# Performance work log

Measured on AMD Instinct MI355X. Metric: run time of the kernel, lower is better.

The kernel has to match this reference:

```python
import jax, jax.numpy as jnp
import numpy as np

S = 3      # num_scales
CIN = 3    # in_channels (hardcoded by expand(...,3,...) in source)
COUT = 3   # out_channels (forced by final broadcast)
K = 3
PAD = 1


def setup_inputs() -> dict:
    key = jax.random.key(0)
    ks = jax.random.split(key, 8)
    B, H, W = 4, 384, 384
    x = jax.random.normal(ks[0], (B, CIN, H, W), jnp.float32)
    # params follow the torch inits: theta,sigma ~ U(0,pi); f0,theta0 = 1
    theta = jax.random.uniform(ks[1], (S, COUT, CIN), jnp.float32) * jnp.pi
    sigma = jax.random.uniform(ks[2], (S, COUT, CIN), jnp.float32) * jnp.pi
    f0 = jnp.ones((S, COUT, CIN), jnp.float32)
    theta0 = jnp.ones((S, COUT, CIN), jnp.float32)
    attn_w1 = jax.random.normal(ks[3], (64, CIN), jnp.float32) * 0.1     # 1x1 conv weight
    attn_b1 = jnp.zeros((64,), jnp.float32)
    attn_w2 = jax.random.normal(ks[4], (COUT * S, 64), jnp.float32) * 0.1
    attn_b2 = jnp.zeros((COUT * S,), jnp.float32)
    conv_w = jax.random.normal(ks[5], (COUT, CIN, K, K), jnp.float32) * 0.05
    mixing = jax.random.uniform(ks[6], (1,), jnp.float32)
    band = jax.random.uniform(ks[7], (COUT, CIN, 2), jnp.float32)        # freq_band_select ~ U(0,1)
    return dict(x=x, theta=theta, sigma=sigma, f0=f0, theta0=theta0,
                attn_w1=attn_w1, attn_b1=attn_b1, attn_w2=attn_w2, attn_b2=attn_b2,
                conv_w=conv_w, mixing=mixing, band=band)


def _log_gabor_bank(theta, sigma, f0, theta0, H, W):
    # vectorized over all scales: returns [S, Co, Cin, H, W] real filter bank
    yy, xx = jnp.meshgrid(jnp.linspace(-1.0, 1.0, H), jnp.linspace(-1.0, 1.0, W), indexing='ij')
    r = jnp.sqrt(xx * xx + yy * yy + 1e-6)          # [H,W]
    phi = jnp.arctan2(yy, xx)                        # [H,W]
    f0e = f0[..., None, None]                        # [S,Co,Cin,1,1]
    sig = sigma[..., None, None]
    th = theta[..., None, None]
    th0 = theta0[..., None, None]
    log_gabor = jnp.exp(-jnp.log(r - jnp.log(f0e)) ** 2 / (2.0 * jnp.log(sig) ** 2))
    angular = jnp.exp(-(phi - th) ** 2 / (2.0 * th0 ** 2))
    return log_gabor * angular


def _forward(x, theta, sigma, f0, theta0, attn_w1, attn_b1, attn_w2, attn_b2, conv_w, mixing, band):
    B, Cin, H, W = x.shape
    # torch.fft.fftshift with no dim shifts ALL axes (incl. batch/channel) -- replicate exactly
    x_freq_shift = jnp.fft.fftshift(jnp.fft.fft2(x))                 # [B,Cin,H,W] complex64

    filt = _log_gabor_bank(theta, sigma, f0, theta0, H, W)           # [S,Co,Cin,H,W]

    # attention net: 1x1 conv -> relu -> 1x1 conv -> softmax over channel dim
    mag = jnp.abs(x_freq_shift)
    h1 = jax.nn.relu(jnp.einsum('bchw,oc->bohw', mag, attn_w1) + attn_b1[None, :, None, None])
    logits = jnp.einsum('bchw,oc->bohw', h1, attn_w2) + attn_b2[None, :, None, None]
    attn = jax.nn.softmax(logits, axis=1).reshape(B, S, COUT, H, W)

    # attended[b,d,h,w] = sum_{s,co} attn[b,s,co,h,w] * xfreq[b,d,h,w] * filt[s,co,d,h,w]
    wgt = jnp.einsum('bschw,scdhw->bdhw', attn, filt)                # real [B,Cin,H,W]
    attended = (x_freq_shift * wgt).sum(axis=1)                      # [B,H,W] complex

    # per-(out,in)-channel square band mask, indices from height (as in source)
    start_idx = jnp.floor((band[..., 0] + 1.0) / 2.0 * H).astype(jnp.int32)   # [Co,Cin]
    end_idx = jnp.floor((band[..., 1] + 1.0) / 2.0 * H).astype(jnp.int32)
    ih = jnp.arange(H)
    rm = (ih[None, None, :] >= start_idx[..., None]) & (ih[None, None, :] < end_idx[..., None])
    iw = jnp.arange(W)
    cm = (iw[None, None, :] >= start_idx[..., None]) & (iw[None, None, :] < end_idx[..., None])
    mask = (rm[..., :, None] & cm[..., None, :]).astype(x.dtype)     # [Co,Cin,H,W]

    # broadcast quirk in source: [B,1,H,W] * [B,Co,1,Cin,H,W] -> [B,Co,B,Cin,H,W]
    six = mask[None, :, None, :, :, :] * attended[None, None, :, None, :, :]
    six = jnp.broadcast_to(six, (B, COUT, B, Cin, H, W))
    # torch ifftshift with no dim shifts ALL 6 axes; ifft2 transforms last two
    x_filtered = jnp.fft.ifft2(jnp.fft.ifftshift(six)).real          # [B,Co,B,Cin,H,W]

    x_spatial = jax.lax.conv_general_dilated(
        x, conv_w, window_strides=(1, 1), padding=[(PAD, PAD), (PAD, PAD)],
        dimension_numbers=('NCHW', 'OIHW', 'NCHW'))                  # [B,Co,H,W]

    mix = mixing[0]
    return mix * x_filtered + (1.0 - mix) * x_spatial[None, None]    # [B,Co,B,Cin,H,W]


def reference(x, theta, sigma, f0, theta0, attn_w1, attn_b1, attn_w2, attn_b2, conv_w, mixing, band):
    return _forward(x, theta, sigma, f0, theta0, attn_w1, attn_b1, attn_w2, attn_b2, conv_w, mixing, band)
```

## Files before the change

kernel.cpp:

```cpp
#include <hip/hip_runtime.h>
#include <math.h>

#define N384 384
#define NPIX 147456
#define LSTRIDE 385
#define LINES 8

__device__ __forceinline__ float2 cmul(float2 a, float2 b) {
    return make_float2(a.x*b.x - a.y*b.y, a.x*b.y + a.y*b.x);
}

template <int NT>
__device__ __forceinline__ void build_tw(float2* tw, int tid) {
    for (int k = tid; k < 384; k += NT) {
        float sn, cs;
        sincospif((float)k * (2.0f / 384.0f), &sn, &cs);
        tw[k] = make_float2(cs, sn);
    }
}

template <int SGNI>
__device__ float2* fft384x8(float2* b0, float2* b1, const float2* tw, int tid) {
    float2* src = b0;
    float2* dst = b1;
    const int line = tid >> 5;
    const int l32  = tid & 31;
    const float SG = (float)SGNI;
    const float s3 = SG * 0.86602540378443864676f;

    {
        float2* L = src + line * LSTRIDE;
        float2* D = dst + line * LSTRIDE;
#pragma unroll
        for (int q = 0; q < 2; ++q) {
            int i = l32 + 32 * q;
            float2 e0 = L[i],       e1 = L[i + 128], e2 = L[i + 256];
            float2 o0 = L[i + 64],  o1 = L[i + 192], o2 = L[i + 320];
            float t1x = e1.x + e2.x, t1y = e1.y + e2.y;
            float t2x = e1.x - e2.x, t2y = e1.y - e2.y;
            float2 E0 = make_float2(e0.x + t1x, e0.y + t1y);
            float mx = e0.x - 0.5f * t1x, my = e0.y - 0.5f * t1y;
            float ux = -s3 * t2y, uy = s3 * t2x;
            float2 E1 = make_float2(mx + ux, my + uy);
            float2 E2 = make_float2(mx - ux, my - uy);
            float s1x = o1.x + o2.x, s1y = o1.y + o2.y;
            float s2x = o1.x - o2.x, s2y = o1.y - o2.y;
            float2 O0 = make_float2(o0.x + s1x, o0.y + s1y);
            float nx = o0.x - 0.5f * s1x, ny = o0.y - 0.5f * s1y;
            float vx = -s3 * s2y, vy = s3 * s2x;
            float2 O1 = make_float2(nx + vx, ny + vy);
            float2 O2 = make_float2(nx - vx, ny - vy);
            float2 T1 = make_float2(0.5f * O1.x - s3 * O1.y, 0.5f * O1.y + s3 * O1.x);
            float2 T2 = make_float2(-0.5f * O2.x - s3 * O2.y, -0.5f * O2.y + s3 * O2.x);
            float2 y0 = make_float2(E0.x + O0.x, E0.y + O0.y);
            float2 y3 = make_float2(E0.x - O0.x, E0.y - O0.y);
            float2 y1 = make_float2(E1.x + T1.x, E1.y + T1.y);
            float2 y4 = make_float2(E1.x - T1.x, E1.y - T1.y);
            float2 y2 = make_float2(E2.x + T2.x, E2.y + T2.y);
            float2 y5 = make_float2(E2.x - T2.x, E2.y - T2.y);
            float2 c1 = tw[i], c2 = tw[2 * i], c3 = tw[3 * i], c4 = tw[4 * i], c5 = tw[5 * i];
            int o = 6 * i;
            D[o]     = y0;
            D[o + 1] = cmul(y1, make_float2(c1.x, SG * c1.y));
            D[o + 2] = cmul(y2, make_float2(c2.x, SG * c2.y));
            D[o + 3] = cmul(y3, make_float2(c3.x, SG * c3.y));
            D[o + 4] = cmul(y4, make_float2(c4.x, SG * c4.y));
            D[o + 5] = cmul(y5, make_float2(c5.x, SG * c5.y));
        }
    }
    __syncthreads();
    { float2* t = src; src = dst; dst = t; }

#pragma unroll
    for (int st = 0; st < 2; ++st) {
        const int s = (st == 0) ? 6 : 24;
        float2* L = src + line * LSTRIDE;
        float2* D = dst + line * LSTRIDE;
#pragma unroll
        for (int q = 0; q < 3; ++q) {
            int i = l32 + 32 * q;
            int k = i % s;
            int js = i - k;
            float2 A0 = L[i];
            float2 A1 = L[i + 96];
            float2 A2 = L[i + 192];
            float2 A3 = L[i + 288];
            float t0x = A0.x + A2.x, t0y = A0.y + A2.y;
            float t1x = A0.x - A2.x, t1y = A0.y - A2.y;
            float t2x = A1.x + A3.x, t2y = A1.y + A3.y;
            float t3x = A1.x - A3.x, t3y = A1.y - A3.y;
            float u3x = -SG * t3y,   u3y = SG * t3x;
            float2 y0 = make_float2(t0x + t2x, t0y + t2y);
            float2 y2 = make_float2(t0x - t2x, t0y - t2y);
            float2 y1 = make_float2(t1x + u3x, t1y + u3y);
            float2 y3 = make_float2(t1x - u3x, t1y - u3y);
            float2 c1 = tw[js], c2 = tw[2 * js], c3 = tw[3 * js];
            float2 w1 = make_float2(c1.x, SG * c1.y);
            float2 w2 = make_float2(c2.x, SG * c2.y);
            float2 w3 = make_float2(c3.x, SG * c3.y);
            int o = i + 3 * js;
            D[o]         = y0;
            D[o + s]     = cmul(y1, w1);
            D[o + 2 * s] = cmul(y2, w2);
            D[o + 3 * s] = cmul(y3, w3);
        }
        __syncthreads();
        { float2* t = src; src = dst; dst = t; }
    }

    {
        float2* L = src + line * LSTRIDE;
        float2* D = dst + line * LSTRIDE;
#pragma unroll
        for (int q = 0; q < 3; ++q) {
            int i = l32 + 32 * q;
            float2 A0 = L[i];
            float2 A1 = L[i + 96];
            float2 A2 = L[i + 192];
            float2 A3 = L[i + 288];
            float t0x = A0.x + A2.x, t0y = A0.y + A2.y;
            float t1x = A0.x - A2.x, t1y = A0.y - A2.y;
            float t2x = A1.x + A3.x, t2y = A1.y + A3.y;
            float t3x = A1.x - A3.x, t3y = A1.y - A3.y;
            float u3x = -SG * t3y,   u3y = SG * t3x;
            D[i]       = make_float2(t0x + t2x, t0y + t2y);
            D[i + 96]  = make_float2(t1x + u3x, t1y + u3y);
            D[i + 192] = make_float2(t0x - t2x, t0y - t2y);
            D[i + 288] = make_float2(t1x - u3x, t1y - u3y);
        }
    }
    __syncthreads();
    return dst;
}

__global__ __launch_bounds__(256) void k_fwd_rows(const float* __restrict__ x,
                                                  float2* __restrict__ F1) {
    __shared__ float2 sbuf[2][LINES * LSTRIDE];
    __shared__ float2 tw[384];
    int img = blockIdx.y;
    int rg  = blockIdx.x;
    int tid = threadIdx.x;
    build_tw<256>(tw, tid);
    const float4* xim = (const float4*)(x + (size_t)img * NPIX + (size_t)rg * 16 * 384);
    for (int idx4 = tid; idx4 < 1536; idx4 += 256) {
        int row = idx4 / 96;
        int e   = (idx4 - row * 96) * 4;
        float4 v = xim[idx4];
        float* L = (float*)(sbuf[0] + (row >> 1) * LSTRIDE + e) + (row & 1);
        L[0] = v.x; L[2] = v.y; L[4] = v.z; L[6] = v.w;
    }
    __syncthreads();
    float2* res = fft384x8<-1>(sbuf[0], sbuf[1], tw, tid);
    float2* F1b = F1 + (size_t)img * NPIX + (size_t)rg * 16 * 384;
    for (int it = tid; it < 1536; it += 256) {
        int line = it / 192;
        int k2   = it - line * 192;
        const float2* L = res + line * LSTRIDE;
        float2 A = L[k2];
        int m = (k2 == 0) ? 0 : 384 - k2;
        float2 B = L[m];
        float2 X1 = make_float2(0.5f * (A.x + B.x), 0.5f * (A.y - B.y));
        float2 X2 = make_float2(0.5f * (A.y + B.y), 0.5f * (B.x - A.x));
        F1b[(size_t)(2 * line) * 384 + k2]     = X1;
        F1b[(size_t)(2 * line + 1) * 384 + k2] = X2;
    }
}

__global__ __launch_bounds__(256) void k_fwd_cols(const float2* __restrict__ In,
                                                  float2* __restrict__ Out) {
    __shared__ float2 sbuf[2][LINES * LSTRIDE];
    __shared__ float2 tw[384];
    int img = blockIdx.y;
    int cg  = blockIdx.x;
    int tid = threadIdx.x;
    build_tw<256>(tw, tid);
    const float4* inim = (const float4*)(In + (size_t)img * NPIX + cg * 8);
    int c = tid & 3, hb = tid >> 2;
    for (int q = 0; q < 6; ++q) {
        int h = hb + 64 * q;
        float4 v = inim[(size_t)h * 192 + c];
        sbuf[0][(2 * c) * LSTRIDE + h]     = make_float2(v.x, v.y);
        sbuf[0][(2 * c + 1) * LSTRIDE + h] = make_float2(v.z, v.w);
    }
    __syncthreads();
    float2* res = fft384x8<-1>(sbuf[0], sbuf[1], tw, tid);
    float4* outim = (float4*)(Out + (size_t)img * NPIX + cg * 8);
    for (int q = 0; q < 3; ++q) {
        int h = hb + 64 * q;
        float2 a = res[(2 * c) * LSTRIDE + h];
        float2 b = res[(2 * c + 1) * LSTRIDE + h];
        outim[(size_t)h * 192 + c] = make_float4(a.x, a.y, b.x, b.y);
    }
}

__global__ __launch_bounds__(192) void k_attn(const float2* __restrict__ F2,
                                              const float* __restrict__ theta,
                                              const float* __restrict__ sigma,
                                              const float* __restrict__ f0,
                                              const float* __restrict__ theta0,
                                              const float* __restrict__ aw1,
                                              const float* __restrict__ ab1,
                                              const float* __restrict__ aw2,
                                              const float* __restrict__ ab2,
                                              const float* __restrict__ band,
                                              float2* __restrict__ A) {
    __shared__ float4 par[27];
    int tid = threadIdx.x;
    if (tid < 27) {
        float lf0 = logf(f0[tid]);
        float ls  = logf(sigma[tid]);
        float na  = -0.5f / (ls * ls);
        float th  = theta[tid];
        float t0  = theta0[tid];
        float nb  = -0.5f / (t0 * t0);
        par[tid] = make_float4(lf0, na, th, nb);
    }
    __syncthreads();

    int h = 192 + blockIdx.x;
    int w = 192 + tid;

    bool needed = false;
#pragma unroll
    for (int q = 0; q < 9; ++q) {
        int s = (int)floorf((band[2 * q + 0] + 1.0f) * 0.5f * 384.0f);
        int e = (int)floorf((band[2 * q + 1] + 1.0f) * 0.5f * 384.0f);
        needed |= (h >= s) && (h < e) && (w >= s) && (w < e);
    }
    if (__ballot(needed) == 0ULL) return;

    int hs = h - 192;
    int ws = w - 192;

    float2 xf[4][3];
    float  mag[4][3];
#pragma unroll
    for (int b = 0; b < 4; ++b) {
        int bp = (b + 2) & 3;
#pragma unroll
        for (int c = 0; c < 3; ++c) {
            int cp = c + 2; if (cp >= 3) cp -= 3;
            float2 v = F2[(size_t)(bp * 3 + cp) * NPIX + (size_t)hs * 384 + ws];
            xf[b][c]  = v;
            mag[b][c] = sqrtf(v.x * v.x + v.y * v.y);
        }
    }

    float lgt[4][9];
#pragma unroll
    for (int b = 0; b < 4; ++b)
#pragma unroll
        for (int j = 0; j < 9; ++j) lgt[b][j] = ab2[j];
    for (int o = 0; o < 64; ++o) {
        float w0 = aw1[o * 3 + 0], w1 = aw1[o * 3 + 1], w2 = aw1[o * 3 + 2];
        float bb = ab1[o];
        float hv[4];
#pragma unroll
        for (int b = 0; b < 4; ++b)
            hv[b] = fmaxf(bb + w0 * mag[b][0] + w1 * mag[b][1] + w2 * mag[b][2], 0.0f);
#pragma unroll
        for (int j = 0; j < 9; ++j) {
            float wj = aw2[j * 64 + o];
#pragma unroll
            for (int b = 0; b < 4; ++b) lgt[b][j] += wj * hv[b];
        }
    }

    float yy = -1.0f + 2.0f * (float)h / 383.0f;
    float xx = -1.0f + 2.0f * (float)w / 383.0f;
    float r   = sqrtf(xx * xx + yy * yy + 1e-6f);
    float phi = atan2f(yy, xx);
    float filt[27];
#pragma unroll
    for (int i = 0; i < 27; ++i) {
        float4 pr = par[i];
        float lr = logf(r - pr.x);
        float dphi = phi - pr.z;
        filt[i] = expf(lr * lr * pr.y + dphi * dphi * pr.w);
    }

#pragma unroll
    for (int b = 0; b < 4; ++b) {
        float mxv = lgt[b][0];
#pragma unroll
        for (int j = 1; j < 9; ++j) mxv = fmaxf(mxv, lgt[b][j]);
        float e[9];
        float se = 0.0f;
#pragma unroll
        for (int j = 0; j < 9; ++j) { e[j] = expf(lgt[b][j] - mxv); se += e[j]; }
        float inv = 1.0f / se;

        float2 acc = make_float2(0.0f, 0.0f);
#pragma unroll
        for (int d = 0; d < 3; ++d) {
            float wg = 0.0f;
#pragma unroll
            for (int s = 0; s < 3; ++s)
#pragma unroll
                for (int co = 0; co < 3; ++co)
                    wg += e[s * 3 + co] * filt[(s * 3 + co) * 3 + d];
            wg *= inv;
            acc.x += xf[b][d].x * wg;
            acc.y += xf[b][d].y * wg;
        }
        if (needed)
            A[(size_t)b * NPIX + (size_t)h * 384 + w] = acc;
    }
}

__global__ __launch_bounds__(256) void k_masked_rows(const float2* __restrict__ A,
                                                     const float* __restrict__ band,
                                                     float2* __restrict__ G1c) {
    int ii  = blockIdx.y;
    int rg  = blockIdx.x;
    int cop = ii / 12;
    int bp  = (ii / 3) % 4;
    int dp  = ii % 3;
    int pidx = (cop * 3 + dp) * 2;
    int sidx = (int)floorf((band[pidx + 0] + 1.0f) * 0.5f * 384.0f);
    int eidx = (int)floorf((band[pidx + 1] + 1.0f) * 0.5f * 384.0f);
    if (eidx <= sidx) return;
    int h0 = 192 + rg * 8;
    if (h0 + 8 <= sidx || h0 >= eidx) return;

    __shared__ float2 sbuf[2][LINES * LSTRIDE];
    __shared__ float2 tw[384];
    int tid = threadIdx.x;
    build_tw<256>(tw, tid);
    const float2* Ab = A + (size_t)bp * NPIX;
    for (int idx = tid; idx < 8 * 384; idx += 256) {
        int line = idx / 384;
        int w    = idx - line * 384;
        int h    = h0 + line;
        bool m = (h >= sidx) && (h < eidx) && (w >= sidx) && (w < eidx);
        float2 v = make_float2(0.0f, 0.0f);
        if (m) v = Ab[(size_t)h * 384 + w];
        sbuf[0][line * LSTRIDE + w] = v;
    }
    __syncthreads();
    float2* res = fft384x8<1>(sbuf[0], sbuf[1], tw, tid);
    for (int idx = tid; idx < 8 * 384; idx += 256) {
        int line = idx / 384;
        int w    = idx - line * 384;
        int h    = h0 + line;
        if (h >= sidx && h < eidx) {
            float2 v = res[line * LSTRIDE + w];
            if (w & 1) { v.x = -v.x; v.y = -v.y; }
            G1c[((size_t)ii * 192 + (h - sidx)) * 384 + w] = v;
        }
    }
}

__global__ __launch_bounds__(128) void k_col_gemm_combine(const float2* __restrict__ G1c,
                                                          const float* __restrict__ band,
                                                          const float* __restrict__ x,
                                                          const float* __restrict__ cw,
                                                          const float* __restrict__ mixing,
                                                          float* __restrict__ out) {
    __shared__ float2 tw[384];
    int tid = threadIdx.x;
    build_tw<128>(tw, tid);

    int ii  = blockIdx.y;
    int gt  = blockIdx.x * 128 + tid;
    int wq  = gt % 96;
    int hg  = gt / 96;
    int w   = wq * 4;
    int h0  = hg * 4;

    int cop = ii / 12;
    int bp  = (ii / 3) % 4;
    int dp  = ii % 3;
    int pidx = (cop * 3 + dp) * 2;
    int sidx = (int)floorf((band[pidx + 0] + 1.0f) * 0.5f * 384.0f);
    int eidx = (int)floorf((band[pidx + 1] + 1.0f) * 0.5f * 384.0f);
    __syncthreads();

    float acc[4][4];
#pragma unroll
    for (int kh = 0; kh < 4; ++kh)
#pragma unroll
        for (int j = 0; j < 4; ++j) acc[kh][j] = 0.0f;

    float2 t[4], rot[4];
#pragma unroll
    for (int kh = 0; kh < 4; ++kh) {
        int h = h0 + kh;
        t[kh]   = tw[(sidx * h) % 384];
        rot[kh] = tw[h];
    }

    const float4* g = (const float4*)(G1c + (size_t)ii * 192 * 384 + w);
    for (int hp = sidx; hp < eidx; ++hp) {
        float4 g0 = g[(size_t)(hp - sidx) * 192];
        float4 g1 = g[(size_t)(hp - sidx) * 192 + 1];
#pragma unroll
        for (int kh = 0; kh < 4; ++kh) {
            float tx = t[kh].x, ty = t[kh].y;
            acc[kh][0] += tx * g0.x - ty * g0.y;
            acc[kh][1] += tx * g0.z - ty * g0.w;
            acc[kh][2] += tx * g1.x - ty * g1.y;
            acc[kh][3] += tx * g1.z - ty * g1.w;
            t[kh] = make_float2(tx * rot[kh].x - ty * rot[kh].y,
                                tx * rot[kh].y + ty * rot[kh].x);
        }
    }

    int co = cop + 2; if (co >= 3) co -= 3;
    int b  = (bp + 2) & 3;
    int d  = dp + 2;  if (d >= 3) d -= 3;

    float cacc[4][4];
#pragma unroll
    for (int kh = 0; kh < 4; ++kh)
#pragma unroll
        for (int j = 0; j < 4; ++j) cacc[kh][j] = 0.0f;
    const float* xb = x + (size_t)b * 3 * NPIX;
#pragma unroll
    for (int ci = 0; ci < 3; ++ci) {
        const float* xc = xb + (size_t)ci * NPIX;
        const float* w9 = cw + ((size_t)d * 3 + ci) * 9;
        float wv[9];
#pragma unroll
        for (int tt = 0; tt < 9; ++tt) wv[tt] = w9[tt];
#pragma unroll
        for (int ihh = 0; ihh < 6; ++ihh) {
            int hh = h0 - 1 + ihh;
            if (hh < 0 || hh >= 384) continue;
            float v[6];
#pragma unroll
            for (int c6 = 0; c6 < 6; ++c6) {
                int ww = w - 1 + c6;
                v[c6] = (ww >= 0 && ww < 384) ? xc[(size_t)hh * 384 + ww] : 0.0f;
            }
#pragma unroll
            for (int kh = 0; kh < 4; ++kh) {
                int r = ihh - kh;
                if (r < 0 || r > 2) continue;
#pragma unroll
                for (int j = 0; j < 4; ++j)
#pragma unroll
                    for (int kw = 0; kw < 3; ++kw)
                        cacc[kh][j] += v[j + kw] * wv[r * 3 + kw];
            }
        }
    }

    float mix  = mixing[0];
    float omix = 1.0f - mix;
    const float invn2 = 1.0f / 147456.0f;
    float* obase = out + (size_t)(co * 12 + b * 3 + d) * NPIX;
#pragma unroll
    for (int kh = 0; kh < 4; ++kh) {
        int h = h0 + kh;
        float sgn = (h & 1) ? -invn2 : invn2;
        size_t off = (size_t)h * 384 + w;
        float4 val;
        val.x = mix * (acc[kh][0] * sgn) + omix * cacc[kh][0];
        val.y = mix * (acc[kh][1] * sgn) + omix * cacc[kh][1];
        val.z = mix * (acc[kh][2] * sgn) + omix * cacc[kh][2];
        val.w = mix * (acc[kh][3] * sgn) + omix * cacc[kh][3];
#pragma unroll
        for (int a = 0; a < 4; ++a)
            *(float4*)(obase + off + (size_t)a * 5308416) = val;
    }
}

extern "C" void kernel_launch(void* const* d_in, const int* in_sizes, int n_in,
                              void* d_out, int out_size, void* d_ws, size_t ws_size,
                              hipStream_t stream) {
    const float* x      = (const float*)d_in[0];
    const float* theta  = (const float*)d_in[1];
    const float* sigma  = (const float*)d_in[2];
    const float* f0     = (const float*)d_in[3];
    const float* theta0 = (const float*)d_in[4];
    const float* aw1    = (const float*)d_in[5];
    const float* ab1    = (const float*)d_in[6];
    const float* aw2    = (const float*)d_in[7];
    const float* ab2    = (const float*)d_in[8];
    const float* cw     = (const float*)d_in[9];
    const float* mixing = (const float*)d_in[10];
    const float* band   = (const float*)d_in[11];
    float* out = (float*)d_out;

    float2* F1  = (float2*)d_ws;
    float2* F2  = F1 + (size_t)12 * NPIX;
    float2* G1c = (float2*)d_ws;
    float2* A   = (float2*)d_ws + (size_t)36 * NPIX;

    k_fwd_rows<<<dim3(24, 12), 256, 0, stream>>>(x, F1);
    k_fwd_cols<<<dim3(24, 12), 256, 0, stream>>>(F1, F2);
    k_attn<<<192, 192, 0, stream>>>(F2, theta, sigma, f0, theta0,
                                    aw1, ab1, aw2, ab2, band, A);
    k_masked_rows<<<dim3(24, 36), 256, 0, stream>>>(A, band, G1c);
    k_col_gemm_combine<<<dim3(72, 36), 128, 0, stream>>>(G1c, band, x, cw, mixing, out);
}
```

Before: 201.2 us.

## Split column DFT reduction across four thread groups with shared-memory combine

The column inverse-DFT loop over the masked band rows is split into four chunks, each handled by a separate 64-thread group, with partial 4x4 accumulators reduced through shared memory. Each thread then finalizes and writes only one output row, with the 3x3 conv also reduced to one row per thread. Launch size doubles to 256 threads and twice the blocks, raising parallelism and shortening the serial dependent loop. The cost is extra shared memory, a barrier, and recomputed conv row loads.

```diff
diff --git a/kernel.cpp b/kernel.cpp
--- a/kernel.cpp
+++ b/kernel.cpp
@@ -351,18 +351,22 @@
     }
 }
 
-__global__ __launch_bounds__(128) void k_col_gemm_combine(const float2* __restrict__ G1c,
+__global__ __launch_bounds__(256) void k_col_gemm_combine(const float2* __restrict__ G1c,
                                                           const float* __restrict__ band,
                                                           const float* __restrict__ x,
                                                           const float* __restrict__ cw,
                                                           const float* __restrict__ mixing,
                                                           float* __restrict__ out) {
     __shared__ float2 tw[384];
+    __shared__ float part[4 * 64 * 17];
     int tid = threadIdx.x;
-    build_tw<128>(tw, tid);
+    build_tw<256>(tw, tid);
+
+    int q   = tid >> 6;
+    int pix = tid & 63;
 
     int ii  = blockIdx.y;
-    int gt  = blockIdx.x * 128 + tid;
+    int gt  = blockIdx.x * 64 + pix;
     int wq  = gt % 96;
     int hg  = gt / 96;
     int w   = wq * 4;
@@ -374,6 +378,10 @@
     int pidx = (cop * 3 + dp) * 2;
     int sidx = (int)floorf((band[pidx + 0] + 1.0f) * 0.5f * 384.0f);
     int eidx = (int)floorf((band[pidx + 1] + 1.0f) * 0.5f * 384.0f);
+    int L = eidx - sidx; if (L < 0) L = 0;
+    int chunk = (L + 3) >> 2;
+    int myS = sidx + q * chunk;
+    int myE = myS + chunk; if (myE > eidx) myE = eidx;
     __syncthreads();
 
     float acc[4][4];
@@ -382,88 +390,92 @@
 #pragma unroll
         for (int j = 0; j < 4; ++j) acc[kh][j] = 0.0f;
 
-    float2 t[4], rot[4];
-#pragma unroll
-    for (int kh = 0; kh < 4; ++kh) {
-        int h = h0 + kh;
-        t[kh]   = tw[(sidx * h) % 384];
-        rot[kh] = tw[h];
-    }
-
-    const float4* g = (const float4*)(G1c + (size_t)ii * 192 * 384 + w);
-    for (int hp = sidx; hp < eidx; ++hp) {
-        float4 g0 = g[(size_t)(hp - sidx) * 192];
-        float4 g1 = g[(size_t)(hp - sidx) * 192 + 1];
+    if (myE > myS) {
+        float2 t[4], rot[4];
 #pragma unroll
         for (int kh = 0; kh < 4; ++kh) {
-            float tx = t[kh].x, ty = t[kh].y;
-            acc[kh][0] += tx * g0.x - ty * g0.y;
-            acc[kh][1] += tx * g0.z - ty * g0.w;
-            acc[kh][2] += tx * g1.x - ty * g1.y;
-            acc[kh][3] += tx * g1.z - ty * g1.w;
-            t[kh] = make_float2(tx * rot[kh].x - ty * rot[kh].y,
-                                tx * rot[kh].y + ty * rot[kh].x);
-        }
+            int h = h0 + kh;
+            t[kh]   = tw[(myS * h) % 384];
+            rot[kh] = tw[h];
+        }
+        const float4* g = (const float4*)(G1c + (size_t)ii * 192 * 384 + w);
+        for (int hp = myS; hp < myE; ++hp) {
+            float4 g0 = g[(size_t)(hp - sidx) * 192];
+            float4 g1 = g[(size_t)(hp - sidx) * 192 + 1];
+#pragma unroll
+            for (int kh = 0; kh < 4; ++kh) {
+                float tx = t[kh].x, ty = t[kh].y;
+                acc[kh][0] += tx * g0.x - ty * g0.y;
+                acc[kh][1] += tx * g0.z - ty * g0.w;
+                acc[kh][2] += tx * g1.x - ty * g1.y;
+                acc[kh][3] += tx * g1.z - ty * g1.w;
+                t[kh] = make_float2(tx * rot[kh].x - ty * rot[kh].y,
+                                    tx * rot[kh].y + ty * rot[kh].x);
+            }
+        }
+    }
+
+    float* mypart = part + (q * 64 + pix) * 17;
+#pragma unroll
+    for (int kh = 0; kh < 4; ++kh)
+#pragma unroll
+        for (int j = 0; j < 4; ++j) mypart[kh * 4 + j] = acc[kh][j];
+    __syncthreads();
+    float fin[4];
+#pragma unroll
+    for (int j = 0; j < 4; ++j) {
+        fin[j] = part[(0 * 64 + pix) * 17 + q * 4 + j]
+               + part[(1 * 64 + pix) * 17 + q * 4 + j]
+               + part[(2 * 64 + pix) * 17 + q * 4 + j]
+               + part[(3 * 64 + pix) * 17 + q * 4 + j];
     }
 
     int co = cop + 2; if (co >= 3) co -= 3;
     int b  = (bp + 2) & 3;
     int d  = dp + 2;  if (d >= 3) d -= 3;
 
-    float cacc[4][4];
-#pragma unroll
-    for (int kh = 0; kh < 4; ++kh)
-#pragma unroll
-        for (int j = 0; j < 4; ++j) cacc[kh][j] = 0.0f;
+    int h = h0 + q;
+    float cacc[4];
+#pragma unroll
+    for (int j = 0; j < 4; ++j) cacc[j] = 0.0f;
     const float* xb = x + (size_t)b * 3 * NPIX;
 #pragma unroll
     for (int ci = 0; ci < 3; ++ci) {
         const float* xc = xb + (size_t)ci * NPIX;
         const float* w9 = cw + ((size_t)d * 3 + ci) * 9;
-        float wv[9];
-#pragma unroll
-        for (int tt = 0; tt < 9; ++tt) wv[tt] = w9[tt];
-#pragma unroll
-        for (int ihh = 0; ihh < 6; ++ihh) {
-            int hh = h0 - 1 + ihh;
+#pragma unroll
+        for (int kh = 0; kh < 3; ++kh) {
+            int hh = h + kh - 1;
             if (hh < 0 || hh >= 384) continue;
+            const float* xr = xc + (size_t)hh * 384;
             float v[6];
 #pragma unroll
             for (int c6 = 0; c6 < 6; ++c6) {
                 int ww = w - 1 + c6;
-                v[c6] = (ww >= 0 && ww < 384) ? xc[(size_t)hh * 384 + ww] : 0.0f;
+                v[c6] = (ww >= 0 && ww < 384) ? xr[ww] : 0.0f;
             }
 #pragma unroll
-            for (int kh = 0; kh < 4; ++kh) {
-                int r = ihh - kh;
-                if (r < 0 || r > 2) continue;
-#pragma unroll
-                for (int j = 0; j < 4; ++j)
-#pragma unroll
-                    for (int kw = 0; kw < 3; ++kw)
-                        cacc[kh][j] += v[j + kw] * wv[r * 3 + kw];
-            }
+            for (int j = 0; j < 4; ++j)
+#pragma unroll
+                for (int kw = 0; kw < 3; ++kw)
+                    cacc[j] += v[j + kw] * w9[kh * 3 + kw];
         }
     }
 
     float mix  = mixing[0];
     float omix = 1.0f - mix;
     const float invn2 = 1.0f / 147456.0f;
+    float sgn = (h & 1) ? -invn2 : invn2;
     float* obase = out + (size_t)(co * 12 + b * 3 + d) * NPIX;
-#pragma unroll
-    for (int kh = 0; kh < 4; ++kh) {
-        int h = h0 + kh;
-        float sgn = (h & 1) ? -invn2 : invn2;
-        size_t off = (size_t)h * 384 + w;
-        float4 val;
-        val.x = mix * (acc[kh][0] * sgn) + omix * cacc[kh][0];
-        val.y = mix * (acc[kh][1] * sgn) + omix * cacc[kh][1];
-        val.z = mix * (acc[kh][2] * sgn) + omix * cacc[kh][2];
-        val.w = mix * (acc[kh][3] * sgn) + omix * cacc[kh][3];
-#pragma unroll
-        for (int a = 0; a < 4; ++a)
-            *(float4*)(obase + off + (size_t)a * 5308416) = val;
-    }
+    size_t off = (size_t)h * 384 + w;
+    float4 val;
+    val.x = mix * (fin[0] * sgn) + omix * cacc[0];
+    val.y = mix * (fin[1] * sgn) + omix * cacc[1];
+    val.z = mix * (fin[2] * sgn) + omix * cacc[2];
+    val.w = mix * (fin[3] * sgn) + omix * cacc[3];
+#pragma unroll
+    for (int a = 0; a < 4; ++a)
+        *(float4*)(obase + off + (size_t)a * 5308416) = val;
 }
 
 extern "C" void kernel_launch(void* const* d_in, const int* in_sizes, int n_in,
@@ -493,5 +505,5 @@
     k_attn<<<192, 192, 0, stream>>>(F2, theta, sigma, f0, theta0,
                                     aw1, ab1, aw2, ab2, band, A);
     k_masked_rows<<<dim3(24, 36), 256, 0, stream>>>(A, band, G1c);
-    k_col_gemm_combine<<<dim3(72, 36), 128, 0, stream>>>(G1c, band, x, cw, mixing, out);
-}
+    k_col_gemm_combine<<<dim3(144, 36), 256, 0, stream>>>(G1c, band, x, cw, mixing, out);
+}
```

Result: slower. 224.3 us (+11.5%).

## Retile column DFT-GEMM to 12 rows per thread with software-pipelined loads

Applied to the files above, without the earlier changes.

Each thread of the column-DFT-plus-combine kernel now computes 12 output rows (strided by 32) over a 16-column strip per block instead of a 4x4 tile, so each loaded G1c row is reused across three times as many twiddle accumulators. The row loads are double-buffered (prefetch two rows ahead) to hide global-memory latency, and the 3x3 conv is recomputed per output row with the weights hoisted into registers. The grid shrinks from 72 to 24 blocks in x, which raises register pressure (48 accumulators plus 24 twiddle registers) and lowers occupancy and block count.

```diff
diff --git a/kernel.cpp b/kernel.cpp
--- a/kernel.cpp
+++ b/kernel.cpp
@@ -361,12 +361,11 @@
     int tid = threadIdx.x;
     build_tw<128>(tw, tid);
 
+    int wt  = blockIdx.x;
     int ii  = blockIdx.y;
-    int gt  = blockIdx.x * 128 + tid;
-    int wq  = gt % 96;
-    int hg  = gt / 96;
-    int w   = wq * 4;
-    int h0  = hg * 4;
+    int wq4 = tid & 3;
+    int hg  = tid >> 2;
+    int w   = wt * 16 + wq4 * 4;
 
     int cop = ii / 12;
     int bp  = (ii / 3) % 4;
@@ -376,33 +375,60 @@
     int eidx = (int)floorf((band[pidx + 1] + 1.0f) * 0.5f * 384.0f);
     __syncthreads();
 
-    float acc[4][4];
-#pragma unroll
-    for (int kh = 0; kh < 4; ++kh)
-#pragma unroll
-        for (int j = 0; j < 4; ++j) acc[kh][j] = 0.0f;
-
-    float2 t[4], rot[4];
-#pragma unroll
-    for (int kh = 0; kh < 4; ++kh) {
-        int h = h0 + kh;
-        t[kh]   = tw[(sidx * h) % 384];
-        rot[kh] = tw[h];
-    }
-
-    const float4* g = (const float4*)(G1c + (size_t)ii * 192 * 384 + w);
-    for (int hp = sidx; hp < eidx; ++hp) {
-        float4 g0 = g[(size_t)(hp - sidx) * 192];
-        float4 g1 = g[(size_t)(hp - sidx) * 192 + 1];
-#pragma unroll
-        for (int kh = 0; kh < 4; ++kh) {
-            float tx = t[kh].x, ty = t[kh].y;
-            acc[kh][0] += tx * g0.x - ty * g0.y;
-            acc[kh][1] += tx * g0.z - ty * g0.w;
-            acc[kh][2] += tx * g1.x - ty * g1.y;
-            acc[kh][3] += tx * g1.z - ty * g1.w;
-            t[kh] = make_float2(tx * rot[kh].x - ty * rot[kh].y,
-                                tx * rot[kh].y + ty * rot[kh].x);
+    float acc[12][4];
+#pragma unroll
+    for (int k = 0; k < 12; ++k)
+#pragma unroll
+        for (int j = 0; j < 4; ++j) acc[k][j] = 0.0f;
+
+    int L = eidx - sidx;
+    if (L > 0) {
+        float2 t[12], rot[12];
+#pragma unroll
+        for (int k = 0; k < 12; ++k) {
+            int h = hg + 32 * k;
+            t[k]   = tw[(sidx * h) % 384];
+            rot[k] = tw[h];
+        }
+        const float4* g = (const float4*)(G1c + (size_t)ii * 192 * 384 + w);
+
+        float4 pa0, pa1, pb0, pb1;
+        {
+            int r0 = 0;
+            int r1 = (1 < L) ? 1 : (L - 1);
+            pa0 = g[(size_t)r0 * 192]; pa1 = g[(size_t)r0 * 192 + 1];
+            pb0 = g[(size_t)r1 * 192]; pb1 = g[(size_t)r1 * 192 + 1];
+        }
+        for (int base = 0; base < L; base += 2) {
+            int r2 = base + 2; r2 = (r2 < L) ? r2 : (L - 1);
+            int r3 = base + 3; r3 = (r3 < L) ? r3 : (L - 1);
+            float4 na0 = g[(size_t)r2 * 192], na1 = g[(size_t)r2 * 192 + 1];
+            float4 nb0 = g[(size_t)r3 * 192], nb1 = g[(size_t)r3 * 192 + 1];
+            {
+#pragma unroll
+                for (int k = 0; k < 12; ++k) {
+                    float tx = t[k].x, ty = t[k].y;
+                    acc[k][0] += tx * pa0.x - ty * pa0.y;
+                    acc[k][1] += tx * pa0.z - ty * pa0.w;
+                    acc[k][2] += tx * pa1.x - ty * pa1.y;
+                    acc[k][3] += tx * pa1.z - ty * pa1.w;
+                    t[k] = make_float2(tx * rot[k].x - ty * rot[k].y,
+                                       tx * rot[k].y + ty * rot[k].x);
+                }
+            }
+            if (base + 1 < L) {
+#pragma unroll
+                for (int k = 0; k < 12; ++k) {
+                    float tx = t[k].x, ty = t[k].y;
+                    acc[k][0] += tx * pb0.x - ty * pb0.y;
+                    acc[k][1] += tx * pb0.z - ty * pb0.w;
+                    acc[k][2] += tx * pb1.x - ty * pb1.y;
+                    acc[k][3] += tx * pb1.z - ty * pb1.w;
+                    t[k] = make_float2(tx * rot[k].x - ty * rot[k].y,
+                                       tx * rot[k].y + ty * rot[k].x);
+                }
+            }
+            pa0 = na0; pa1 = na1; pb0 = nb0; pb1 = nb1;
         }
     }
 
@@ -410,56 +436,53 @@
     int b  = (bp + 2) & 3;
     int d  = dp + 2;  if (d >= 3) d -= 3;
 
-    float cacc[4][4];
-#pragma unroll
-    for (int kh = 0; kh < 4; ++kh)
-#pragma unroll
-        for (int j = 0; j < 4; ++j) cacc[kh][j] = 0.0f;
-    const float* xb = x + (size_t)b * 3 * NPIX;
-#pragma unroll
-    for (int ci = 0; ci < 3; ++ci) {
-        const float* xc = xb + (size_t)ci * NPIX;
-        const float* w9 = cw + ((size_t)d * 3 + ci) * 9;
-        float wv[9];
-#pragma unroll
-        for (int tt = 0; tt < 9; ++tt) wv[tt] = w9[tt];
-#pragma unroll
-        for (int ihh = 0; ihh < 6; ++ihh) {
-            int hh = h0 - 1 + ihh;
-            if (hh < 0 || hh >= 384) continue;
-            float v[6];
-#pragma unroll
-            for (int c6 = 0; c6 < 6; ++c6) {
-                int ww = w - 1 + c6;
-                v[c6] = (ww >= 0 && ww < 384) ? xc[(size_t)hh * 384 + ww] : 0.0f;
-            }
-#pragma unroll
-            for (int kh = 0; kh < 4; ++kh) {
-                int r = ihh - kh;
-                if (r < 0 || r > 2) continue;
-#pragma unroll
-                for (int j = 0; j < 4; ++j)
-#pragma unroll
-                    for (int kw = 0; kw < 3; ++kw)
-                        cacc[kh][j] += v[j + kw] * wv[r * 3 + kw];
-            }
-        }
-    }
+    float wv[3][9];
+#pragma unroll
+    for (int ci = 0; ci < 3; ++ci)
+#pragma unroll
+        for (int tt = 0; tt < 9; ++tt) wv[ci][tt] = cw[((size_t)d * 3 + ci) * 9 + tt];
 
     float mix  = mixing[0];
     float omix = 1.0f - mix;
     const float invn2 = 1.0f / 147456.0f;
+    const float* xb = x + (size_t)b * 3 * NPIX;
     float* obase = out + (size_t)(co * 12 + b * 3 + d) * NPIX;
-#pragma unroll
-    for (int kh = 0; kh < 4; ++kh) {
-        int h = h0 + kh;
+
+#pragma unroll
+    for (int k = 0; k < 12; ++k) {
+        int h = hg + 32 * k;
+        float cacc[4];
+#pragma unroll
+        for (int j = 0; j < 4; ++j) cacc[j] = 0.0f;
+#pragma unroll
+        for (int ci = 0; ci < 3; ++ci) {
+            const float* xc = xb + (size_t)ci * NPIX;
+#pragma unroll
+            for (int kh = 0; kh < 3; ++kh) {
+                int hh = h + kh - 1;
+                if (hh < 0 || hh >= 384) continue;
+                const float* xr = xc + (size_t)hh * 384;
+                float v[6];
+#pragma unroll
+                for (int c6 = 0; c6 < 6; ++c6) {
+                    int ww = w - 1 + c6;
+                    v[c6] = (ww >= 0 && ww < 384) ? xr[ww] : 0.0f;
+                }
+#pragma unroll
+                for (int j = 0; j < 4; ++j)
+#pragma unroll
+                    for (int kw = 0; kw < 3; ++kw)
+                        cacc[j] += v[j + kw] * wv[ci][kh * 3 + kw];
+            }
+        }
+
         float sgn = (h & 1) ? -invn2 : invn2;
         size_t off = (size_t)h * 384 + w;
         float4 val;
-        val.x = mix * (acc[kh][0] * sgn) + omix * cacc[kh][0];
-        val.y = mix * (acc[kh][1] * sgn) + omix * cacc[kh][1];
-        val.z = mix * (acc[kh][2] * sgn) + omix * cacc[kh][2];
-        val.w = mix * (acc[kh][3] * sgn) + omix * cacc[kh][3];
+        val.x = mix * (acc[k][0] * sgn) + omix * cacc[0];
+        val.y = mix * (acc[k][1] * sgn) + omix * cacc[1];
+        val.z = mix * (acc[k][2] * sgn) + omix * cacc[2];
+        val.w = mix * (acc[k][3] * sgn) + omix * cacc[3];
 #pragma unroll
         for (int a = 0; a < 4; ++a)
             *(float4*)(obase + off + (size_t)a * 5308416) = val;
@@ -493,5 +516,5 @@
     k_attn<<<192, 192, 0, stream>>>(F2, theta, sigma, f0, theta0,
                                     aw1, ab1, aw2, ab2, band, A);
     k_masked_rows<<<dim3(24, 36), 256, 0, stream>>>(A, band, G1c);
-    k_col_gemm_combine<<<dim3(72, 36), 128, 0, stream>>>(G1c, band, x, cw, mixing, out);
-}
+    k_col_gemm_combine<<<dim3(24, 36), 128, 0, stream>>>(G1c, band, x, cw, mixing, out);
+}
```

Measured after the change: 303.9 us. 51.0% more time.
